# Performance work log

Hardware: AMD Instinct MI355X
Metric: run time of the kernel (lower is better)

Reference implementation:

```python
import jax, jax.numpy as jnp
import numpy as np

BATCH = 32
N_LEVELS = (16384, 4096, 1024, 256)   # nodes at each mesh resolution
M_LEVELS = (4096, 1024, 256, 64)      # nodes after each Pool (downsample)
DEG = 6                               # directed edges per node
POOL_K = 3                            # nnz per row of downsample matrix
FILTERS = (3, 32, 32, 32, 64)         # channel chain of the 4 ChebConvs
K_CHEB = 6                            # Chebyshev polynomial order


def setup_inputs() -> dict:
    key = jax.random.key(0)
    ks = iter(jax.random.split(key, 64))
    inp = {"x": jax.random.normal(next(ks), (BATCH, N_LEVELS[0], FILTERS[0]), jnp.float32)}
    for i, N in enumerate(N_LEVELS):
        er = jnp.repeat(jnp.arange(N), DEG)
        off = jax.random.randint(next(ks), (N * DEG,), 1, N)
        inp[f"er{i}"] = er
        inp[f"ec{i}"] = (er + off) % N  # guaranteed no self loops
    for i, (M, N) in enumerate(zip(M_LEVELS, N_LEVELS)):
        inp[f"pr{i}"] = jnp.repeat(jnp.arange(M), POOL_K)
        inp[f"pc{i}"] = jax.random.randint(next(ks), (M * POOL_K,), 0, N)
        inp[f"pv{i}"] = jax.random.uniform(next(ks), (M * POOL_K,), jnp.float32)
    for i in range(4):
        fin, fout = FILTERS[i], FILTERS[i + 1]
        scale = 1.0 / np.sqrt(fin * K_CHEB)
        inp[f"W{i}"] = jax.random.normal(next(ks), (K_CHEB, fin, fout), jnp.float32) * scale
        inp[f"b{i}"] = jnp.zeros((fout,), jnp.float32)
    inp["enc_W"] = jax.random.normal(next(ks), (M_LEVELS[-1] * FILTERS[-1], 128), jnp.float32) * 0.1
    inp["enc_b"] = jnp.zeros((128,), jnp.float32)
    inp["cls_W"] = jax.random.normal(next(ks), (128, 10), jnp.float32) * 0.1
    inp["cls_b"] = jnp.zeros((10,), jnp.float32)
    return inp


def _cheb_conv(x, er, ec, W, b):
    # x: [B,N,Fin]; W: [K,Fin,Fout].
    # PyG ChebConv with lambda_max=2: L_hat = L - I = -D^{-1/2} A D^{-1/2}.
    N = x.shape[1]
    deg = jnp.zeros((N,), x.dtype).at[er].add(1.0)
    dinv = jnp.where(deg > 0, 1.0 / jnp.sqrt(jnp.maximum(deg, 1.0)), 0.0)
    norm = -(dinv[er] * dinv[ec])  # [E]

    def L(t):  # sparse matvec: gather neighbor feats, weight, scatter-add
        return jnp.zeros_like(t).at[:, er].add(t[:, ec] * norm[None, :, None])

    Tx0 = x
    out = jnp.einsum("bnf,fg->bng", Tx0, W[0])
    Tx1 = L(x)
    out = out + jnp.einsum("bnf,fg->bng", Tx1, W[1])
    for k in range(2, W.shape[0]):
        Tx2 = 2.0 * L(Tx1) - Tx0
        out = out + jnp.einsum("bnf,fg->bng", Tx2, W[k])
        Tx0, Tx1 = Tx1, Tx2
    return out + b


def _pool(x, pr, pc, pv, m):
    # sparse downsample matrix [m,N]: index_select cols * value, scatter_add rows
    B, _, F = x.shape
    return jnp.zeros((B, m, F), x.dtype).at[:, pr].add(x[:, pc] * pv[None, :, None])


def reference(x, er0, ec0, er1, ec1, er2, ec2, er3, ec3,
              pr0, pc0, pv0, pr1, pc1, pv1, pr2, pc2, pv2, pr3, pc3, pv3,
              W0, b0, W1, b1, W2, b2, W3, b3, enc_W, enc_b, cls_W, cls_b):
    ers, ecs = (er0, er1, er2, er3), (ec0, ec1, ec2, ec3)
    prs, pcs, pvs = (pr0, pr1, pr2, pr3), (pc0, pc1, pc2, pc3), (pv0, pv1, pv2, pv3)
    Ws, bs = (W0, W1, W2, W3), (b0, b1, b2, b3)
    for i in range(4):  # fixed n_layers loop (structurally distinct layers)
        x = jax.nn.relu(_cheb_conv(x, ers[i], ecs[i], Ws[i], bs[i]))
        x = _pool(x, prs[i], pcs[i], pvs[i], M_LEVELS[i])
    x = x.reshape(x.shape[0], -1)  # [B, 64*64]
    h = jax.nn.relu(x @ enc_W + enc_b)
    return h @ cls_W + cls_b
```

## Files before the change

kernel.cpp:

```cpp
#include <hip/hip_runtime.h>
#include <hip/hip_fp16.h>
#include <cstddef>
#include <cstdint>

#define BATCH 32


struct alignas(8) half4 { __half2 lo, hi; };

__device__ __forceinline__ void h4f(const half4 h, float f[4]) {
  float2 a = __half22float2(h.lo);
  float2 c = __half22float2(h.hi);
  f[0] = a.x; f[1] = a.y; f[2] = c.x; f[3] = c.y;
}
__device__ __forceinline__ void fma4(float4& a, float s, const float4& w) {
  a.x += s * w.x; a.y += s * w.y; a.z += s * w.z; a.w += s * w.w;
}
__device__ __forceinline__ float4 relu4(const float4& a) {
  return make_float4(fmaxf(a.x, 0.f), fmaxf(a.y, 0.f), fmaxf(a.z, 0.f), fmaxf(a.w, 0.f));
}

__global__ void __launch_bounds__(256) transpose_h(
    const float* __restrict__ x, half4* __restrict__ xh)
{
  int t = blockIdx.x * 256 + threadIdx.x;
  int n = t >> 5;
  int b = t & 31;
  const float* src = x + ((size_t)b * 16384 + n) * 3;
  half4 h;
  h.lo = __floats2half2_rn(src[0], src[1]);
  h.hi = __floats2half2_rn(src[2], 0.f);
  xh[t] = h;
}

template<int N>
__global__ void __launch_bounds__(256) cheb_step_h(
    const half4* __restrict__ Tin, const half4* __restrict__ Tpp,
    const int* __restrict__ ec, half4* __restrict__ Tout,
    float coef, float beta)
{
  int idx = blockIdx.x * 256 + threadIdx.x;
  int n = idx >> 5;
  int b = idx & 31;
  const int* e = ec + n * 6;
  float s0 = 0.f, s1 = 0.f, s2 = 0.f;
#pragma unroll
  for (int d = 0; d < 6; ++d) {
    half4 v = Tin[(e[d] << 5) | b];
    float2 a = __half22float2(v.lo);
    float2 c = __half22float2(v.hi);
    s0 += a.x; s1 += a.y; s2 += c.x;
  }
  half4 p = Tpp[idx];
  float2 pa = __half22float2(p.lo);
  float2 pc = __half22float2(p.hi);
  half4 o;
  o.lo = __floats2half2_rn(coef * s0 + beta * pa.x, coef * s1 + beta * pa.y);
  o.hi = __floats2half2_rn(coef * s2 + beta * pc.x, 0.f);
  Tout[idx] = o;
}

template<int N, int M, int FOUT>
__global__ void __launch_bounds__(256) pool_conv_f3_h(
    const half4* __restrict__ Xh, const half4* __restrict__ T,
    const float* __restrict__ W, const float* __restrict__ bias,
    const int* __restrict__ pc, const float* __restrict__ pv,
    float* __restrict__ out)
{
  constexpr int F4 = FOUT / 4;
  constexpr size_t SL = (size_t)N * 32;
  __shared__ float Ws[6 * 3 * FOUT];
  for (int i = threadIdx.x; i < 6 * 3 * FOUT; i += 256) Ws[i] = W[i];
  __syncthreads();
  const float4* Ws4 = (const float4*)Ws;
  int t = blockIdx.x * 256 + threadIdx.x;
  int fo4 = t % F4;
  int b   = (t / F4) % BATCH;
  int m   = t / (F4 * BATCH);
  int c0 = pc[m * 3 + 0], c1 = pc[m * 3 + 1], c2 = pc[m * 3 + 2];
  float v0 = pv[m * 3 + 0], v1 = pv[m * 3 + 1], v2 = pv[m * 3 + 2];
  float4 bi = ((const float4*)bias)[fo4];
  float4 a0 = bi, a1 = bi, a2 = bi;
#pragma unroll
  for (int k = 0; k < 6; ++k) {
    const half4* base = (k == 0) ? Xh : (T + (size_t)(k - 1) * SL);
    float r0[4], r1[4], r2[4];
    h4f(base[(c0 << 5) | b], r0);
    h4f(base[(c1 << 5) | b], r1);
    h4f(base[(c2 << 5) | b], r2);
#pragma unroll
    for (int f = 0; f < 3; ++f) {
      float4 w = Ws4[(k * 3 + f) * F4 + fo4];
      fma4(a0, r0[f], w);
      fma4(a1, r1[f], w);
      fma4(a2, r2[f], w);
    }
  }
  a0 = relu4(a0); a1 = relu4(a1); a2 = relu4(a2);
  float4 acc;
  acc.x = v0*a0.x + v1*a1.x + v2*a2.x;
  acc.y = v0*a0.y + v1*a1.y + v2*a2.y;
  acc.z = v0*a0.z + v1*a1.z + v2*a2.z;
  acc.w = v0*a0.w + v1*a1.w + v2*a2.w;
  ((float4*)out)[((size_t)m * BATCH + b) * F4 + fo4] = acc;
}

template<int N, int F, int THREADS, int MINW>
__global__ void __launch_bounds__(THREADS, MINW) cheb_recur_h4(
    const float* __restrict__ X,
    const int* __restrict__ ec,
    __half* __restrict__ Th)
{
  constexpr int NPT = N / THREADS;
  __shared__ float4 cur[N];
  const float cI = -1.0f / 6.0f;
  const float cS = -1.0f / 3.0f;
  const int b = blockIdx.x & 31;
  const int fbase = (blockIdx.x >> 5) * 4;
  constexpr size_t SLH = (size_t)N * 32 * F;
  float4 prevv[NPT];
#pragma unroll
  for (int i = 0; i < NPT; ++i) {
    int n = threadIdx.x + i * THREADS;
    cur[n] = *(const float4*)(X + ((size_t)n * 32 + b) * F + fbase);
  }
  __syncthreads();
#pragma unroll 1
  for (int k = 1; k <= 5; ++k) {
    float4 newv[NPT];
    __half* Tk = Th + (size_t)(k - 1) * SLH;
#pragma unroll
    for (int i = 0; i < NPT; ++i) {
      int n = threadIdx.x + i * THREADS;
      const int* e = ec + n * 6;
      float4 s = make_float4(0.f, 0.f, 0.f, 0.f);
#pragma unroll
      for (int d = 0; d < 6; ++d) {
        float4 t = cur[e[d]];
        s.x += t.x; s.y += t.y; s.z += t.z; s.w += t.w;
      }
      float4 v;
      if (k == 1) {
        v.x = cI * s.x; v.y = cI * s.y; v.z = cI * s.z; v.w = cI * s.w;
      } else {
        v.x = cS * s.x - prevv[i].x; v.y = cS * s.y - prevv[i].y;
        v.z = cS * s.z - prevv[i].z; v.w = cS * s.w - prevv[i].w;
      }
      newv[i] = v;
      half4 h;
      h.lo = __floats2half2_rn(v.x, v.y);
      h.hi = __floats2half2_rn(v.z, v.w);
      *(half4*)(Tk + ((size_t)n * 32 + b) * F + fbase) = h;
    }
    __syncthreads();
#pragma unroll
    for (int i = 0; i < NPT; ++i) {
      int n = threadIdx.x + i * THREADS;
      prevv[i] = cur[n];
      cur[n] = newv[i];
    }
    __syncthreads();
  }
}

template<int N, int M, int FOUT, bool OUT_BM>
__global__ void __launch_bounds__(256) pool_conv_v32_h(
    const float* __restrict__ X, const __half* __restrict__ Th,
    const float* __restrict__ W, const float* __restrict__ bias,
    const int* __restrict__ pc, const float* __restrict__ pv,
    float* __restrict__ out)
{
  constexpr int FIN = 32;
  constexpr int F4 = FOUT / 4;
  constexpr size_t SLH = (size_t)N * 32 * FIN;
  __shared__ float Ws[6 * FIN * FOUT];
  for (int i = threadIdx.x; i < 6 * FIN * FOUT; i += 256) Ws[i] = W[i];
  __syncthreads();
  const float4* Ws4 = (const float4*)Ws;
  const float4* X4p = (const float4*)X;
  int t = blockIdx.x * 256 + threadIdx.x;
  int fo4 = t % F4;
  int b   = (t / F4) % BATCH;
  int m   = t / (F4 * BATCH);
  int c0 = pc[m * 3 + 0], c1 = pc[m * 3 + 1], c2 = pc[m * 3 + 2];
  float v0 = pv[m * 3 + 0], v1 = pv[m * 3 + 1], v2 = pv[m * 3 + 2];
  float4 bi = ((const float4*)bias)[fo4];
  float4 a0 = bi, a1 = bi, a2 = bi;
  {
    const float4* r0 = X4p + ((size_t)c0 * BATCH + b) * 8;
    const float4* r1 = X4p + ((size_t)c1 * BATCH + b) * 8;
    const float4* r2 = X4p + ((size_t)c2 * BATCH + b) * 8;
#pragma unroll
    for (int fi = 0; fi < 8; ++fi) {
      float4 t0 = r0[fi], t1 = r1[fi], t2 = r2[fi];
#pragma unroll
      for (int ff = 0; ff < 4; ++ff) {
        float4 w = Ws4[(fi * 4 + ff) * F4 + fo4];
        fma4(a0, ((const float*)&t0)[ff], w);
        fma4(a1, ((const float*)&t1)[ff], w);
        fma4(a2, ((const float*)&t2)[ff], w);
      }
    }
  }
#pragma unroll 1
  for (int k = 1; k < 6; ++k) {
    const half4* base = (const half4*)(Th + (size_t)(k - 1) * SLH);
    const half4* r0 = base + ((size_t)c0 * 32 + b) * 8;
    const half4* r1 = base + ((size_t)c1 * 32 + b) * 8;
    const half4* r2 = base + ((size_t)c2 * 32 + b) * 8;
#pragma unroll
    for (int q = 0; q < 8; ++q) {
      float f0[4], f1[4], f2[4];
      h4f(r0[q], f0); h4f(r1[q], f1); h4f(r2[q], f2);
#pragma unroll
      for (int ff = 0; ff < 4; ++ff) {
        float4 w = Ws4[((k * 32) + q * 4 + ff) * F4 + fo4];
        fma4(a0, f0[ff], w);
        fma4(a1, f1[ff], w);
        fma4(a2, f2[ff], w);
      }
    }
  }
  a0 = relu4(a0); a1 = relu4(a1); a2 = relu4(a2);
  float4 acc;
  acc.x = v0*a0.x + v1*a1.x + v2*a2.x;
  acc.y = v0*a0.y + v1*a1.y + v2*a2.y;
  acc.z = v0*a0.z + v1*a1.z + v2*a2.z;
  acc.w = v0*a0.w + v1*a1.w + v2*a2.w;
  size_t oi = OUT_BM ? (((size_t)b * M + m) * F4 + fo4) : (((size_t)m * BATCH + b) * F4 + fo4);
  ((float4*)out)[oi] = acc;
}

__global__ void __launch_bounds__(256) encoder_partial(
    const float* __restrict__ Xf, const float* __restrict__ encW,
    float* __restrict__ partial)
{
  int b  = blockIdx.x;
  int ks = blockIdx.y;
  int fo = threadIdx.x & 127;
  int half = threadIdx.x >> 7;
  const float* xr = Xf + b * 4096 + ks * 256 + half * 128;
  const float* w  = encW + (size_t)(ks * 256 + half * 128) * 128;
  float acc = 0.f;
#pragma unroll 8
  for (int i = 0; i < 128; ++i) acc += xr[i] * w[(size_t)i * 128 + fo];
  __shared__ float part[256];
  part[threadIdx.x] = acc;
  __syncthreads();
  if (half == 0) partial[(size_t)(b * 16 + ks) * 128 + fo] = part[fo] + part[128 + fo];
}

__global__ void __launch_bounds__(128) encoder_reduce_cls(
    const float* __restrict__ partial, const float* __restrict__ encB,
    const float* __restrict__ clsW, const float* __restrict__ clsB,
    float* __restrict__ out)
{
  int b = blockIdx.x;
  int fo = threadIdx.x;
  float acc = encB[fo];
#pragma unroll
  for (int ks = 0; ks < 16; ++ks) acc += partial[(size_t)(b * 16 + ks) * 128 + fo];
  __shared__ float Hs[128];
  Hs[fo] = fmaxf(acc, 0.f);
  __syncthreads();
  if (fo < 10) {
    float s = clsB[fo];
#pragma unroll 4
    for (int f = 0; f < 128; ++f) s += Hs[f] * clsW[f * 10 + fo];
    out[b * 10 + fo] = s;
  }
}

extern "C" void kernel_launch(void* const* d_in, const int* in_sizes, int n_in,
                              void* d_out, int out_size, void* d_ws, size_t ws_size,
                              hipStream_t stream)
{
  const float* x   = (const float*)d_in[0];
  const int* ec0 = (const int*)d_in[2];
  const int* ec1 = (const int*)d_in[4];
  const int* ec2 = (const int*)d_in[6];
  const int* ec3 = (const int*)d_in[8];
  const int* pc0 = (const int*)d_in[10]; const float* pv0 = (const float*)d_in[11];
  const int* pc1 = (const int*)d_in[13]; const float* pv1 = (const float*)d_in[14];
  const int* pc2 = (const int*)d_in[16]; const float* pv2 = (const float*)d_in[17];
  const int* pc3 = (const int*)d_in[19]; const float* pv3 = (const float*)d_in[20];
  const float* W0 = (const float*)d_in[21]; const float* b0 = (const float*)d_in[22];
  const float* W1 = (const float*)d_in[23]; const float* b1 = (const float*)d_in[24];
  const float* W2 = (const float*)d_in[25]; const float* b2 = (const float*)d_in[26];
  const float* W3 = (const float*)d_in[27]; const float* b3 = (const float*)d_in[28];
  const float* encW = (const float*)d_in[29]; const float* encB = (const float*)d_in[30];
  const float* clsW = (const float*)d_in[31]; const float* clsB = (const float*)d_in[32];
  float* out = (float*)d_out;

  float* ws = (float*)d_ws;
  half4*  Xh = (half4*)ws;
  __half* Th = (__half*)(ws + 1048576);
  float* X1 = ws + 1048576 + 10485760;
  float* X2 = X1 + 4194304;
  float* X3 = X2 + 1048576;
  float* X4 = X3 + 262144;
  float* P  = X4 + 131072;

  const float cI = -1.0f / 6.0f;
  const float cS = -1.0f / 3.0f;
  dim3 blk(256);

  transpose_h<<<dim3(2048), blk, 0, stream>>>(x, Xh);

  {
    constexpr size_t S = (size_t)16384 * 32;
    half4* T4 = (half4*)Th;
    cheb_step_h<16384><<<dim3(2048), blk, 0, stream>>>(Xh,       Xh,       ec0, T4,        cI,  0.f);
    cheb_step_h<16384><<<dim3(2048), blk, 0, stream>>>(T4,       Xh,       ec0, T4 + S,    cS, -1.f);
    cheb_step_h<16384><<<dim3(2048), blk, 0, stream>>>(T4 + S,   T4,       ec0, T4 + 2*S,  cS, -1.f);
    cheb_step_h<16384><<<dim3(2048), blk, 0, stream>>>(T4 + 2*S, T4 + S,   ec0, T4 + 3*S,  cS, -1.f);
    cheb_step_h<16384><<<dim3(2048), blk, 0, stream>>>(T4 + 3*S, T4 + 2*S, ec0, T4 + 4*S,  cS, -1.f);
    pool_conv_f3_h<16384, 4096, 32><<<dim3(4096), blk, 0, stream>>>(
        Xh, (const half4*)Th, W0, b0, pc0, pv0, X1);
  }
  {
    cheb_recur_h4<4096, 32, 1024, 4><<<dim3(256), dim3(1024), 0, stream>>>(X1, ec1, Th);
    pool_conv_v32_h<4096, 1024, 32, false><<<dim3(1024), blk, 0, stream>>>(
        X1, Th, W1, b1, pc1, pv1, X2);
  }
  {
    cheb_recur_h4<1024, 32, 256, 4><<<dim3(256), blk, 0, stream>>>(X2, ec2, Th);
    pool_conv_v32_h<1024, 256, 32, false><<<dim3(256), blk, 0, stream>>>(
        X2, Th, W2, b2, pc2, pv2, X3);
  }
  {
    cheb_recur_h4<256, 32, 256, 4><<<dim3(256), blk, 0, stream>>>(X3, ec3, Th);
    pool_conv_v32_h<256, 64, 64, true><<<dim3(128), blk, 0, stream>>>(
        X3, Th, W3, b3, pc3, pv3, X4);
  }
  encoder_partial<<<dim3(32, 16), blk, 0, stream>>>(X4, encW, P);
  encoder_reduce_cls<<<dim3(32), dim3(128), 0, stream>>>(P, encB, clsW, clsB, out);
}
```

Baseline: 278.3 us.

## Halve cheb_step blocks, store recurrence state in fp16 LDS, restructure encoder

Result: no change. 281.7 us (+1.2%).

```diff
diff --git a/kernel.cpp b/kernel.cpp
--- a/kernel.cpp
+++ b/kernel.cpp
@@ -33,8 +33,7 @@
   xh[t] = h;
 }
 
-template<int N>
-__global__ void __launch_bounds__(256) cheb_step_h(
+__global__ void __launch_bounds__(256) cheb_step_h2(
     const half4* __restrict__ Tin, const half4* __restrict__ Tpp,
     const int* __restrict__ ec, half4* __restrict__ Tout,
     float coef, float beta)
@@ -42,22 +41,35 @@
   int idx = blockIdx.x * 256 + threadIdx.x;
   int n = idx >> 5;
   int b = idx & 31;
-  const int* e = ec + n * 6;
+  int idx2 = idx + 262144;
+  const int* e  = ec + n * 6;
+  const int* e2 = ec + (n + 8192) * 6;
   float s0 = 0.f, s1 = 0.f, s2 = 0.f;
+  float u0 = 0.f, u1 = 0.f, u2 = 0.f;
 #pragma unroll
   for (int d = 0; d < 6; ++d) {
-    half4 v = Tin[(e[d] << 5) | b];
+    half4 v = Tin[(e[d]  << 5) | b];
+    half4 w = Tin[(e2[d] << 5) | b];
     float2 a = __half22float2(v.lo);
     float2 c = __half22float2(v.hi);
     s0 += a.x; s1 += a.y; s2 += c.x;
-  }
-  half4 p = Tpp[idx];
+    float2 aw = __half22float2(w.lo);
+    float2 cw = __half22float2(w.hi);
+    u0 += aw.x; u1 += aw.y; u2 += cw.x;
+  }
+  half4 p  = Tpp[idx];
+  half4 p2 = Tpp[idx2];
   float2 pa = __half22float2(p.lo);
   float2 pc = __half22float2(p.hi);
-  half4 o;
-  o.lo = __floats2half2_rn(coef * s0 + beta * pa.x, coef * s1 + beta * pa.y);
-  o.hi = __floats2half2_rn(coef * s2 + beta * pc.x, 0.f);
-  Tout[idx] = o;
+  float2 qa = __half22float2(p2.lo);
+  float2 qc = __half22float2(p2.hi);
+  half4 o, o2;
+  o.lo  = __floats2half2_rn(coef * s0 + beta * pa.x, coef * s1 + beta * pa.y);
+  o.hi  = __floats2half2_rn(coef * s2 + beta * pc.x, 0.f);
+  o2.lo = __floats2half2_rn(coef * u0 + beta * qa.x, coef * u1 + beta * qa.y);
+  o2.hi = __floats2half2_rn(coef * u2 + beta * qc.x, 0.f);
+  Tout[idx]  = o;
+  Tout[idx2] = o2;
 }
 
 template<int N, int M, int FOUT>
@@ -106,50 +118,61 @@
 }
 
 template<int N, int F, int THREADS, int MINW>
-__global__ void __launch_bounds__(THREADS, MINW) cheb_recur_h4(
+__global__ void __launch_bounds__(THREADS, MINW) cheb_recur_hh(
     const float* __restrict__ X,
     const int* __restrict__ ec,
     __half* __restrict__ Th)
 {
   constexpr int NPT = N / THREADS;
-  __shared__ float4 cur[N];
+  __shared__ half4 cur[N];
   const float cI = -1.0f / 6.0f;
   const float cS = -1.0f / 3.0f;
   const int b = blockIdx.x & 31;
   const int fbase = (blockIdx.x >> 5) * 4;
   constexpr size_t SLH = (size_t)N * 32 * F;
-  float4 prevv[NPT];
+  half4 prevv[NPT], newh[NPT];
 #pragma unroll
   for (int i = 0; i < NPT; ++i) {
     int n = threadIdx.x + i * THREADS;
-    cur[n] = *(const float4*)(X + ((size_t)n * 32 + b) * F + fbase);
+    float4 xv = *(const float4*)(X + ((size_t)n * 32 + b) * F + fbase);
+    half4 h;
+    h.lo = __floats2half2_rn(xv.x, xv.y);
+    h.hi = __floats2half2_rn(xv.z, xv.w);
+    cur[n] = h;
   }
   __syncthreads();
 #pragma unroll 1
   for (int k = 1; k <= 5; ++k) {
-    float4 newv[NPT];
     __half* Tk = Th + (size_t)(k - 1) * SLH;
 #pragma unroll
     for (int i = 0; i < NPT; ++i) {
       int n = threadIdx.x + i * THREADS;
-      const int* e = ec + n * 6;
-      float4 s = make_float4(0.f, 0.f, 0.f, 0.f);
+      const int2* e2 = (const int2*)(ec + n * 6);
+      int2 ea = e2[0], eb = e2[1], ez = e2[2];
+      int na[6];
+      na[0] = ea.x; na[1] = ea.y; na[2] = eb.x;
+      na[3] = eb.y; na[4] = ez.x; na[5] = ez.y;
+      float s0 = 0.f, s1 = 0.f, s2 = 0.f, s3 = 0.f;
 #pragma unroll
       for (int d = 0; d < 6; ++d) {
-        float4 t = cur[e[d]];
-        s.x += t.x; s.y += t.y; s.z += t.z; s.w += t.w;
+        half4 t = cur[na[d]];
+        float2 a = __half22float2(t.lo);
+        float2 c = __half22float2(t.hi);
+        s0 += a.x; s1 += a.y; s2 += c.x; s3 += c.y;
       }
-      float4 v;
+      float v0, v1, v2, v3;
       if (k == 1) {
-        v.x = cI * s.x; v.y = cI * s.y; v.z = cI * s.z; v.w = cI * s.w;
+        v0 = cI * s0; v1 = cI * s1; v2 = cI * s2; v3 = cI * s3;
       } else {
-        v.x = cS * s.x - prevv[i].x; v.y = cS * s.y - prevv[i].y;
-        v.z = cS * s.z - prevv[i].z; v.w = cS * s.w - prevv[i].w;
+        float2 pa = __half22float2(prevv[i].lo);
+        float2 pc = __half22float2(prevv[i].hi);
+        v0 = cS * s0 - pa.x; v1 = cS * s1 - pa.y;
+        v2 = cS * s2 - pc.x; v3 = cS * s3 - pc.y;
       }
-      newv[i] = v;
       half4 h;
-      h.lo = __floats2half2_rn(v.x, v.y);
-      h.hi = __floats2half2_rn(v.z, v.w);
+      h.lo = __floats2half2_rn(v0, v1);
+      h.hi = __floats2half2_rn(v2, v3);
+      newh[i] = h;
       *(half4*)(Tk + ((size_t)n * 32 + b) * F + fbase) = h;
     }
     __syncthreads();
@@ -157,7 +180,7 @@
     for (int i = 0; i < NPT; ++i) {
       int n = threadIdx.x + i * THREADS;
       prevv[i] = cur[n];
-      cur[n] = newv[i];
+      cur[n] = newh[i];
     }
     __syncthreads();
   }
@@ -231,23 +254,24 @@
   ((float4*)out)[oi] = acc;
 }
 
-__global__ void __launch_bounds__(256) encoder_partial(
+__global__ void __launch_bounds__(128) encoder_partial_ws(
     const float* __restrict__ Xf, const float* __restrict__ encW,
     float* __restrict__ partial)
 {
-  int b  = blockIdx.x;
-  int ks = blockIdx.y;
-  int fo = threadIdx.x & 127;
-  int half = threadIdx.x >> 7;
-  const float* xr = Xf + b * 4096 + ks * 256 + half * 128;
-  const float* w  = encW + (size_t)(ks * 256 + half * 128) * 128;
-  float acc = 0.f;
-#pragma unroll 8
-  for (int i = 0; i < 128; ++i) acc += xr[i] * w[(size_t)i * 128 + fo];
-  __shared__ float part[256];
-  part[threadIdx.x] = acc;
-  __syncthreads();
-  if (half == 0) partial[(size_t)(b * 16 + ks) * 128 + fo] = part[fo] + part[128 + fo];
+  int j  = blockIdx.x;
+  int fo = threadIdx.x;
+  int i0 = j * 32;
+  float w[32];
+#pragma unroll
+  for (int i = 0; i < 32; ++i) w[i] = encW[(size_t)(i0 + i) * 128 + fo];
+#pragma unroll 1
+  for (int b = 0; b < 32; ++b) {
+    const float* xr = Xf + b * 4096 + i0;
+    float s = 0.f;
+#pragma unroll
+    for (int i = 0; i < 32; ++i) s += xr[i] * w[i];
+    partial[((size_t)b * 128 + j) * 128 + fo] = s;
+  }
 }
 
 __global__ void __launch_bounds__(128) encoder_reduce_cls(
@@ -258,8 +282,8 @@
   int b = blockIdx.x;
   int fo = threadIdx.x;
   float acc = encB[fo];
-#pragma unroll
-  for (int ks = 0; ks < 16; ++ks) acc += partial[(size_t)(b * 16 + ks) * 128 + fo];
+#pragma unroll 8
+  for (int j = 0; j < 128; ++j) acc += partial[((size_t)b * 128 + j) * 128 + fo];
   __shared__ float Hs[128];
   Hs[fo] = fmaxf(acc, 0.f);
   __syncthreads();
@@ -310,29 +334,26 @@
   {
     constexpr size_t S = (size_t)16384 * 32;
     half4* T4 = (half4*)Th;
-    cheb_step_h<16384><<<dim3(2048), blk, 0, stream>>>(Xh,       Xh,       ec0, T4,        cI,  0.f);
-    cheb_step_h<16384><<<dim3(2048), blk, 0, stream>>>(T4,       Xh,       ec0, T4 + S,    cS, -1.f);
-    cheb_step_h<16384><<<dim3(2048), blk, 0, stream>>>(T4 + S,   T4,       ec0, T4 + 2*S,  cS, -1.f);
-    cheb_step_h<16384><<<dim3(2048), blk, 0, stream>>>(T4 + 2*S, T4 + S,   ec0, T4 + 3*S,  cS, -1.f);
-    cheb_step_h<16384><<<dim3(2048), blk, 0, stream>>>(T4 + 3*S, T4 + 2*S, ec0, T4 + 4*S,  cS, -1.f);
+    cheb_step_h2<<<dim3(1024), blk, 0, stream>>>(Xh,       Xh,       ec0, T4,        cI,  0.f);
+    cheb_step_h2<<<dim3(1024), blk, 0, stream>>>(T4,       Xh,       ec0, T4 + S,    cS, -1.f);
+    cheb_step_h2<<<dim3(1024), blk, 0, stream>>>(T4 + S,   T4,       ec0, T4 + 2*S,  cS, -1.f);
+    cheb_step_h2<<<dim3(1024), blk, 0, stream>>>(T4 + 2*S, T4 + S,   ec0, T4 + 3*S,  cS, -1.f);
+    cheb_step_h2<<<dim3(1024), blk, 0, stream>>>(T4 + 3*S, T4 + 2*S, ec0, T4 + 4*S,  cS, -1.f);
     pool_conv_f3_h<16384, 4096, 32><<<dim3(4096), blk, 0, stream>>>(
         Xh, (const half4*)Th, W0, b0, pc0, pv0, X1);
   }
-  {
-    cheb_recur_h4<4096, 32, 1024, 4><<<dim3(256), dim3(1024), 0, stream>>>(X1, ec1, Th);
-    pool_conv_v32_h<4096, 1024, 32, false><<<dim3(1024), blk, 0, stream>>>(
-        X1, Th, W1, b1, pc1, pv1, X2);
-  }
-  {
-    cheb_recur_h4<1024, 32, 256, 4><<<dim3(256), blk, 0, stream>>>(X2, ec2, Th);
-    pool_conv_v32_h<1024, 256, 32, false><<<dim3(256), blk, 0, stream>>>(
-        X2, Th, W2, b2, pc2, pv2, X3);
-  }
-  {
-    cheb_recur_h4<256, 32, 256, 4><<<dim3(256), blk, 0, stream>>>(X3, ec3, Th);
-    pool_conv_v32_h<256, 64, 64, true><<<dim3(128), blk, 0, stream>>>(
-        X3, Th, W3, b3, pc3, pv3, X4);
-  }
-  encoder_partial<<<dim3(32, 16), blk, 0, stream>>>(X4, encW, P);
+  cheb_recur_hh<4096, 32, 1024, 4><<<dim3(256), dim3(1024), 0, stream>>>(X1, ec1, Th);
+  pool_conv_v32_h<4096, 1024, 32, false><<<dim3(1024), blk, 0, stream>>>(
+      X1, Th, W1, b1, pc1, pv1, X2);
+
+  cheb_recur_hh<1024, 32, 256, 4><<<dim3(256), blk, 0, stream>>>(X2, ec2, Th);
+  pool_conv_v32_h<1024, 256, 32, false><<<dim3(256), blk, 0, stream>>>(
+      X2, Th, W2, b2, pc2, pv2, X3);
+
+  cheb_recur_hh<256, 32, 256, 4><<<dim3(256), blk, 0, stream>>>(X3, ec3, Th);
+  pool_conv_v32_h<256, 64, 64, true><<<dim3(128), blk, 0, stream>>>(
+      X3, Th, W3, b3, pc3, pv3, X4);
+
+  encoder_partial_ws<<<dim3(128), dim3(128), 0, stream>>>(X4, encW, P);
   encoder_reduce_cls<<<dim3(32), dim3(128), 0, stream>>>(P, encB, clsW, clsB, out);
 }
```
